# Kernel optimization log

Measured on AMD Instinct MI355X. Metric: run time of the kernel, lower is better.

## Reference

```python
import jax, jax.numpy as jnp
import numpy as np

K = 4096
N = 11008
GROUP_SIZE = 128
NUM_GROUPS = K // GROUP_SIZE
BATCH = 4
SEQ = 2048


def setup_inputs() -> dict:
    key = jax.random.key(0)
    kx, kw, ks = jax.random.split(key, 3)
    x = jax.random.normal(kx, (BATCH, SEQ, K), dtype=jnp.float16)
    # packed uint8 bytes, each holding two INT4 values (stored as int32)
    weight_packed = jax.random.randint(kw, (N, K // 2), 0, 256, dtype=jnp.int32)
    # positive group-wise scales ~ abs(randn)*0.1 -> uniform*0.1 is fine statistically
    scales = (jax.random.uniform(ks, (N, NUM_GROUPS), dtype=jnp.float32) * 0.1).astype(jnp.float16)
    return {"x": x, "weight_packed": weight_packed, "scales": scales}


def _dequantize(weight_packed, scales):
    # unpack: low nibble first, then high nibble -> (N, K) values in [0, 15]
    low = weight_packed & 15
    high = (weight_packed >> 4) & 15
    w_int = jnp.stack([low, high], axis=-1).reshape(weight_packed.shape[0], -1)  # (N, K)
    # symmetric dequant with implicit zero-point 8, group-wise scales
    scales_expanded = jnp.repeat(scales, GROUP_SIZE, axis=1)  # (N, K)
    return scales_expanded * (w_int.astype(jnp.float16) - jnp.float16(8.0))


def reference(x, weight_packed, scales):
    # Y = X @ W_dequant.T : (B, S, K) x (N, K) -> (B, S, N)
    w_dequant = _dequantize(weight_packed, scales)  # (N, K) fp16
    out = jnp.einsum('bsk,nk->bsn', x, w_dequant)
    return out.astype(jnp.float16)
```

## Files before the change

kernel.cpp:

```cpp
#include <hip/hip_runtime.h>
#include <stdint.h>


namespace {

typedef unsigned int u32;
typedef unsigned short u16;
typedef __attribute__((ext_vector_type(8))) short bf16x8;
typedef __attribute__((ext_vector_type(4))) float f32x4;
typedef __attribute__((ext_vector_type(4))) u32 u32x4;

constexpr int Mt = 8192;
constexpr int Nt = 11008;
constexpr int Kt = 4096;
constexpr int KP = Kt / 2;
constexpr int NG = 32;
constexpr int BM = 256;
constexpr int BN = 256;
constexpr int BK = 64;
constexpr int THREADS = 512;
constexpr int GRID = (Mt / BM) * (Nt / BN);
constexpr int NKT = Kt / BK;
constexpr int NB_CNT = Nt / BN;

__device__ __forceinline__ u16 f2bf(float f) {
  u32 u = __float_as_uint(f);
  return (u16)((u + 0x7FFFu + ((u >> 16) & 1u)) >> 16);
}
__device__ __forceinline__ u32 pk2bf(float a, float b) {
  return (u32)f2bf(a) | ((u32)f2bf(b) << 16);
}
__device__ __forceinline__ u32 dqpair(u32 b, float s, float c) {
  float f0 = (float)(b & 15u);
  float f1 = (float)((b >> 4) & 15u);
  return pk2bf(fmaf(f0, s, c), fmaf(f1, s, c));
}
__device__ __forceinline__ void async16(const void* g, void* l) {
  __builtin_amdgcn_global_load_lds(
      (const __attribute__((address_space(1))) u32*)g,
      (__attribute__((address_space(3))) u32*)l, 16, 0, 0);
}

__global__ __launch_bounds__(256) void cvt_x(const float* __restrict__ X,
                                             u32* __restrict__ O) {
  const int total = Mt * Kt / 4;
  for (int j = blockIdx.x * 256 + threadIdx.x; j < total;
       j += (int)(gridDim.x * 256)) {
    float4 v = ((const float4*)X)[j];
    ((uint2*)O)[j] = make_uint2(pk2bf(v.x, v.y), pk2bf(v.z, v.w));
  }
}

__global__ __launch_bounds__(256) void cvt_w(const int* __restrict__ W,
                                             const float* __restrict__ S,
                                             u32* __restrict__ O) {
  const int total = Nt * KP / 4;
  for (int j = blockIdx.x * 256 + threadIdx.x; j < total;
       j += (int)(gridDim.x * 256)) {
    int4 v = ((const int4*)W)[j];
    int vv[4] = {v.x, v.y, v.z, v.w};
    const int j0 = j * 4;
    const int row = j0 >> 11;
    const int jj = j0 & 2047;
    const float* sr = S + (size_t)row * NG;
    u32x4 o;
    #pragma unroll
    for (int e = 0; e < 4; ++e) {
      float s = sr[(jj + e) >> 6];
      o[e] = dqpair((u32)vv[e], s, -8.f * s);
    }
    ((u32x4*)O)[j] = o;
  }
}

__global__ __launch_bounds__(THREADS, 2) void gemm8p(
    const u16* __restrict__ Xb, const u16* __restrict__ Wb,
    float* __restrict__ Y) {
  __shared__ __align__(16) unsigned char smem[131072];

  const int tid  = (int)threadIdx.x;
  const int lane = tid & 63;
  const int wid  = tid >> 6;
  const int wm   = wid >> 2;
  const int wn   = wid & 3;

  const int bid = (int)blockIdx.x;
  const int wg  = (bid & 7) * (GRID / 8) + (bid >> 3);
  const int mb  = wg / NB_CNT;
  const int nb  = wg - mb * NB_CNT;
  const int m0  = mb * BM;
  const int n0  = nb * BN;

  const int srow = tid >> 3;
  const int sswz = (tid & 7) ^ (srow & 7);
  const u16* aRow = Xb + (size_t)(m0 + srow) * Kt + sswz * 8;
  const u16* bRow = Wb + (size_t)(n0 + (srow >> 5) * 64 + (srow & 31)) * Kt + sswz * 8;
  const int ldst = tid * 16;

  const int frow = lane & 15;
  const int fk   = lane >> 4;
  const int s0o  = ((fk ^ (lane & 7)) << 4);
  const int s1o  = (((4 + fk) ^ (lane & 7)) << 4);
  const int aRdC = (wm * 64 + frow) * 128;
  const int bRdC = (wn * 32 + frow) * 128;

  f32x4 acc[8][4];
  #pragma unroll
  for (int i = 0; i < 8; ++i)
    #pragma unroll
    for (int j = 0; j < 4; ++j) acc[i][j] = f32x4{0.f, 0.f, 0.f, 0.f};

  #define GATE(n) asm volatile("s_waitcnt vmcnt(" #n ")" ::: "memory")
  #define BAR()   asm volatile("s_barrier" ::: "memory")

  #define STAGE_A(g, buf, kt)                                                  \
    do {                                                                       \
      unsigned char* d_ = smem + (buf) * 32768 + (g) * 16384 + ldst;           \
      const u16* s_ = aRow + (size_t)((g) * 64) * Kt + (kt) * 64;              \
      async16(s_, d_);                                                         \
      async16(s_ + (size_t)128 * Kt, d_ + 8192);                               \
    } while (0)
  #define STAGE_B(p, buf, kt)                                                  \
    do {                                                                       \
      unsigned char* d_ = smem + 65536 + (buf) * 32768 + (p) * 16384 + ldst;   \
      const u16* s_ = bRow + (size_t)((p) * 32) * Kt + (kt) * 64;              \
      async16(s_, d_);                                                         \
      async16(s_ + (size_t)128 * Kt, d_ + 8192);                               \
    } while (0)

  #define LD_A(dst, g, buf)                                                    \
    do {                                                                       \
      const unsigned char* b_ = smem + (buf) * 32768 + (g) * 16384 + aRdC;     \
      _Pragma("unroll")                                                        \
      for (int q_ = 0; q_ < 4; ++q_) {                                         \
        dst[q_][0] = *(const bf16x8*)(b_ + q_ * 2048 + s0o);                   \
        dst[q_][1] = *(const bf16x8*)(b_ + q_ * 2048 + s1o);                   \
      }                                                                        \
    } while (0)
  #define LD_B(dst, p, buf)                                                    \
    do {                                                                       \
      const unsigned char* b_ =                                                \
          smem + 65536 + (buf) * 32768 + (p) * 16384 + bRdC;                   \
      _Pragma("unroll")                                                        \
      for (int q_ = 0; q_ < 2; ++q_) {                                         \
        dst[q_][0] = *(const bf16x8*)(b_ + q_ * 2048 + s0o);                   \
        dst[q_][1] = *(const bf16x8*)(b_ + q_ * 2048 + s1o);                   \
      }                                                                        \
    } while (0)

  #define MM(FG, FNP, A_, B_)                                                  \
    do {                                                                       \
      __builtin_amdgcn_s_setprio(1);                                           \
      _Pragma("unroll")                                                        \
      for (int fm_ = 0; fm_ < 4; ++fm_)                                        \
        _Pragma("unroll")                                                      \
        for (int fn_ = 0; fn_ < 2; ++fn_)                                      \
          _Pragma("unroll")                                                    \
          for (int kk_ = 0; kk_ < 2; ++kk_)                                    \
            acc[(FG) * 4 + fm_][(FNP) * 2 + fn_] =                             \
                __builtin_amdgcn_mfma_f32_16x16x32_bf16(                       \
                    A_[fm_][kk_], B_[fn_][kk_],                                \
                    acc[(FG) * 4 + fm_][(FNP) * 2 + fn_], 0, 0, 0);            \
      __builtin_amdgcn_s_setprio(0);                                           \
    } while (0)

  bf16x8 af[4][2], b0[2][2], b1[2][2];

  STAGE_A(0, 0, 0);
  STAGE_B(0, 0, 0);
  STAGE_A(1, 0, 0);
  STAGE_B(1, 0, 0);
  STAGE_A(0, 1, 1);
  STAGE_B(0, 1, 1);
  STAGE_A(1, 1, 1);

  #pragma unroll 1
  for (int t = 0; t < NKT - 2; ++t) {
    const int b = t & 1;
    GATE(10); BAR();
    LD_A(af, 0, b);
    LD_B(b0, 0, b);
    STAGE_B(1, b ^ 1, t + 1);
    MM(0, 0, af, b0);
    GATE(8); BAR();
    LD_B(b1, 1, b);
    STAGE_A(0, b, t + 2);
    MM(0, 1, af, b1);
    GATE(12); BAR();
    LD_A(af, 1, b);
    STAGE_B(0, b, t + 2);
    MM(1, 0, af, b0);
    BAR();
    STAGE_A(1, b, t + 2);
    MM(1, 1, af, b1);
  }

  {
    GATE(10); BAR();
    LD_A(af, 0, 0);
    LD_B(b0, 0, 0);
    STAGE_B(1, 1, 63);
    MM(0, 0, af, b0);
    GATE(8); BAR();
    LD_B(b1, 1, 0);
    MM(0, 1, af, b1);
    GATE(10); BAR();
    LD_A(af, 1, 0);
    MM(1, 0, af, b0);
    BAR();
    MM(1, 1, af, b1);
  }
  {
    GATE(4); BAR();
    LD_A(af, 0, 1);
    LD_B(b0, 0, 1);
    MM(0, 0, af, b0);
    GATE(0); BAR();
    LD_B(b1, 1, 1);
    MM(0, 1, af, b1);
    BAR();
    LD_A(af, 1, 1);
    MM(1, 0, af, b0);
    MM(1, 1, af, b1);
  }

  #undef GATE
  #undef BAR
  #undef STAGE_A
  #undef STAGE_B
  #undef LD_A
  #undef LD_B
  #undef MM

  #pragma unroll
  for (int fm = 0; fm < 8; ++fm) {
    #pragma unroll
    for (int r = 0; r < 4; ++r) {
      const size_t mrow = (size_t)(m0 + wm * 128 + fm * 16 + fk * 4 + r) * Nt;
      #pragma unroll
      for (int fn = 0; fn < 4; ++fn) {
        Y[mrow + (size_t)(n0 + wn * 64 + fn * 16 + frow)] = acc[fm][fn][r];
      }
    }
  }
}

__global__ __launch_bounds__(512) void gemm_fused(
    const float* __restrict__ Xf, const int* __restrict__ W,
    const float* __restrict__ S, float* __restrict__ Y) {
  constexpr int FBN = 128;
  constexpr int FNB = Nt / FBN;
  constexpr int FBK = 64;
  constexpr int FNKT = Kt / FBK;
  __shared__ __align__(16) unsigned char Alds[BM * FBK * 2];
  __shared__ __align__(16) unsigned char Blds[FBN * FBK * 2];

  const int tid = (int)threadIdx.x;
  const int lane = tid & 63;
  const int wid = tid >> 6;
  const int wm = wid >> 1;
  const int wn = wid & 1;

  const int bid = (int)blockIdx.x;
  const int fgrid = (Mt / BM) * FNB;
  const int wg = (bid & 7) * (fgrid / 8) + (bid >> 3);
  const int mb = wg / FNB;
  const int nb = wg - mb * FNB;
  const int m0 = mb * BM;
  const int n0 = nb * FBN;

  const int frow = lane & 15;
  const int fk = lane >> 4;
  const int fswz = (lane & 7) << 4;
  const unsigned char* aRd = Alds + (wm * 64 + frow) * 128;
  const unsigned char* bRd = Blds + (wn * 64 + frow) * 128;

  f32x4 acc[4][4];
  #pragma unroll
  for (int i = 0; i < 4; ++i)
    #pragma unroll
    for (int j = 0; j < 4; ++j) acc[i][j] = f32x4{0.f, 0.f, 0.f, 0.f};

  const int arow = tid >> 3, acol = tid & 7;
  const float* fA = Xf + (size_t)(m0 + arow) * Kt + acol * 8;
  unsigned char* fAD = Alds + arow * 128 + ((acol ^ (arow & 7)) << 4);
  const int nloc = tid >> 3, c4 = tid & 7;
  const int* fB0 = W + (size_t)(n0 + nloc) * KP + c4 * 4;
  const int* fB1 = fB0 + (size_t)64 * KP;
  const float* sp0 = S + (size_t)(n0 + nloc) * NG;
  const float* sp1 = sp0 + (size_t)64 * NG;
  unsigned char* fBD0 = Blds + nloc * 128 + ((c4 ^ (nloc & 7)) << 4);
  unsigned char* fBD1 = fBD0 + 64 * 128;

  #pragma unroll 1
  for (int kt = 0; kt < FNKT; ++kt) {
    const int k0 = kt * FBK;
    #pragma unroll
    for (int p = 0; p < 4; ++p) {
      float4 x0 = *(const float4*)(fA + (size_t)p * 64 * Kt + k0);
      float4 x1 = *(const float4*)(fA + (size_t)p * 64 * Kt + k0 + 4);
      u32x4 q;
      q[0] = pk2bf(x0.x, x0.y); q[1] = pk2bf(x0.z, x0.w);
      q[2] = pk2bf(x1.x, x1.y); q[3] = pk2bf(x1.z, x1.w);
      *(u32x4*)(fAD + p * 64 * 128) = q;
    }
    const int g = k0 >> 7;
    const float s0 = sp0[g], s1 = sp1[g];
    const float c0 = -8.f * s0, c1 = -8.f * s1;
    const int4 w0 = *(const int4*)(fB0 + (k0 >> 1));
    const int4 w1 = *(const int4*)(fB1 + (k0 >> 1));
    u32x4 q0, q1;
    q0[0] = dqpair((u32)w0.x, s0, c0); q0[1] = dqpair((u32)w0.y, s0, c0);
    q0[2] = dqpair((u32)w0.z, s0, c0); q0[3] = dqpair((u32)w0.w, s0, c0);
    q1[0] = dqpair((u32)w1.x, s1, c1); q1[1] = dqpair((u32)w1.y, s1, c1);
    q1[2] = dqpair((u32)w1.z, s1, c1); q1[3] = dqpair((u32)w1.w, s1, c1);
    *(u32x4*)fBD0 = q0;
    *(u32x4*)fBD1 = q1;

    __syncthreads();

    #pragma unroll
    for (int kk = 0; kk < 2; ++kk) {
      const int koff = (kk * 64 + fk * 16) ^ fswz;
      bf16x8 af[4], bfr[4];
      #pragma unroll
      for (int fm = 0; fm < 4; ++fm)
        af[fm] = *(const bf16x8*)(aRd + fm * 16 * 128 + koff);
      #pragma unroll
      for (int fn = 0; fn < 4; ++fn)
        bfr[fn] = *(const bf16x8*)(bRd + fn * 16 * 128 + koff);
      #pragma unroll
      for (int fm = 0; fm < 4; ++fm)
        #pragma unroll
        for (int fn = 0; fn < 4; ++fn)
          acc[fm][fn] = __builtin_amdgcn_mfma_f32_16x16x32_bf16(
              af[fm], bfr[fn], acc[fm][fn], 0, 0, 0);
    }
    __syncthreads();
  }

  #pragma unroll
  for (int fm = 0; fm < 4; ++fm) {
    #pragma unroll
    for (int r = 0; r < 4; ++r) {
      const size_t mrow = (size_t)(m0 + wm * 64 + fm * 16 + fk * 4 + r) * Nt;
      #pragma unroll
      for (int fn = 0; fn < 4; ++fn)
        Y[mrow + (size_t)(n0 + wn * 64 + fn * 16 + frow)] = acc[fm][fn][r];
    }
  }
}

}

extern "C" void kernel_launch(void* const* d_in, const int* in_sizes, int n_in,
                              void* d_out, int out_size, void* d_ws, size_t ws_size,
                              hipStream_t stream) {
  (void)in_sizes; (void)n_in; (void)out_size;
  const float* X = (const float*)d_in[0];
  const int* W   = (const int*)d_in[1];
  const float* S = (const float*)d_in[2];
  float* Y       = (float*)d_out;

  const size_t xbytes = (size_t)Mt * Kt * 2;
  const size_t wbytes = (size_t)Nt * Kt * 2;

  if (ws_size >= xbytes + wbytes) {
    u16* Xb = (u16*)d_ws;
    u16* Wb = (u16*)((char*)d_ws + xbytes);
    cvt_x<<<dim3(2048), dim3(256), 0, stream>>>(X, (u32*)Xb);
    cvt_w<<<dim3(2048), dim3(256), 0, stream>>>(W, S, (u32*)Wb);
    gemm8p<<<dim3(GRID), dim3(THREADS), 0, stream>>>(Xb, Wb, Y);
  } else {
    gemm_fused<<<dim3((Mt / BM) * (Nt / 128)), dim3(512), 0, stream>>>(X, W, S, Y);
  }
}
```

Measured before the change: 706.2 us.

## Restructure GEMM main loop pipeline with per-MFMA-block barriers and reordered staging

Reworks the software pipeline of the bf16 GEMM main loop. Each MFMA block is now bracketed by barriers, scheduling fences and an lgkmcnt(0) wait, and the vmcnt gate is moved to the end of the last block. The order of async global-to-LDS stages is rotated so B tiles are prefetched earlier and A tile 1 later. The aim is a more regular ping-pong between LDS reads, global loads and MFMA work across waves, at the cost of twice as many barriers per iteration and a full LDS-read drain after every MFMA group.

```diff
diff --git a/kernel.cpp b/kernel.cpp
--- a/kernel.cpp
+++ b/kernel.cpp
@@ -111,7 +111,9 @@
     for (int j = 0; j < 4; ++j) acc[i][j] = f32x4{0.f, 0.f, 0.f, 0.f};
 
   #define GATE(n) asm volatile("s_waitcnt vmcnt(" #n ")" ::: "memory")
-  #define BAR()   asm volatile("s_barrier" ::: "memory")
+  #define BARR()  asm volatile("s_barrier" ::: "memory")
+  #define LGK0()  asm volatile("s_waitcnt lgkmcnt(0)" ::: "memory")
+  #define SCH0()  __builtin_amdgcn_sched_barrier(0)
 
   #define STAGE_A(g, buf, kt)                                                  \
     do {                                                                       \
@@ -148,8 +150,10 @@
       }                                                                        \
     } while (0)
 
-  #define MM(FG, FNP, A_, B_)                                                  \
-    do {                                                                       \
+  #define MM_G(FG, FNP, A_, B_, GN)                                            \
+    do {                                                                       \
+      BARR();                                                                  \
+      SCH0();                                                                  \
       __builtin_amdgcn_s_setprio(1);                                           \
       _Pragma("unroll")                                                        \
       for (int fm_ = 0; fm_ < 4; ++fm_)                                        \
@@ -162,75 +166,75 @@
                     A_[fm_][kk_], B_[fn_][kk_],                                \
                     acc[(FG) * 4 + fm_][(FNP) * 2 + fn_], 0, 0, 0);            \
       __builtin_amdgcn_s_setprio(0);                                           \
-    } while (0)
+      SCH0();                                                                  \
+      LGK0();                                                                  \
+      if ((GN) == 6) { asm volatile("s_waitcnt vmcnt(6)" ::: "memory"); }      \
+      else if ((GN) == 0) { asm volatile("s_waitcnt vmcnt(0)" ::: "memory"); } \
+      BARR();                                                                  \
+    } while (0)
+  #define MM(FG, FNP, A_, B_) MM_G(FG, FNP, A_, B_, -1)
 
   bf16x8 af[4][2], b0[2][2], b1[2][2];
 
   STAGE_A(0, 0, 0);
   STAGE_B(0, 0, 0);
+  STAGE_B(1, 0, 0);
   STAGE_A(1, 0, 0);
-  STAGE_B(1, 0, 0);
   STAGE_A(0, 1, 1);
   STAGE_B(0, 1, 1);
-  STAGE_A(1, 1, 1);
+  STAGE_B(1, 1, 1);
+  GATE(6);
+  BARR();
 
   #pragma unroll 1
   for (int t = 0; t < NKT - 2; ++t) {
     const int b = t & 1;
-    GATE(10); BAR();
     LD_A(af, 0, b);
     LD_B(b0, 0, b);
-    STAGE_B(1, b ^ 1, t + 1);
+    STAGE_A(1, b ^ 1, t + 1);
     MM(0, 0, af, b0);
-    GATE(8); BAR();
     LD_B(b1, 1, b);
     STAGE_A(0, b, t + 2);
     MM(0, 1, af, b1);
-    GATE(12); BAR();
     LD_A(af, 1, b);
     STAGE_B(0, b, t + 2);
     MM(1, 0, af, b0);
-    BAR();
-    STAGE_A(1, b, t + 2);
-    MM(1, 1, af, b1);
+    STAGE_B(1, b, t + 2);
+    MM_G(1, 1, af, b1, 6);
   }
 
   {
-    GATE(10); BAR();
     LD_A(af, 0, 0);
     LD_B(b0, 0, 0);
-    STAGE_B(1, 1, 63);
+    STAGE_A(1, 1, 63);
     MM(0, 0, af, b0);
-    GATE(8); BAR();
     LD_B(b1, 1, 0);
     MM(0, 1, af, b1);
-    GATE(10); BAR();
     LD_A(af, 1, 0);
     MM(1, 0, af, b0);
-    BAR();
-    MM(1, 1, af, b1);
+    MM_G(1, 1, af, b1, 0);
   }
   {
-    GATE(4); BAR();
     LD_A(af, 0, 1);
     LD_B(b0, 0, 1);
     MM(0, 0, af, b0);
-    GATE(0); BAR();
     LD_B(b1, 1, 1);
     MM(0, 1, af, b1);
-    BAR();
     LD_A(af, 1, 1);
     MM(1, 0, af, b0);
     MM(1, 1, af, b1);
   }
 
   #undef GATE
-  #undef BAR
+  #undef BARR
+  #undef LGK0
+  #undef SCH0
   #undef STAGE_A
   #undef STAGE_B
   #undef LD_A
   #undef LD_B
   #undef MM
+  #undef MM_G
 
   #pragma unroll
   for (int fm = 0; fm < 8; ++fm) {
```

After: 730.2 us. 3.4% more time.
